# Optimization experiments

Hardware: AMD Instinct MI355X
Metric: run time of the kernel (lower is better)

## Reference

```python
import jax, jax.numpy as jnp
import numpy as np

TOP_K = 2  # moe_top_k


def setup_inputs() -> dict:
    key = jax.random.key(0)
    k0, k1, k2, k3 = jax.random.split(key, 4)
    SL, BS, H, F, E = 2048, 4, 1024, 1024, 8
    x = jax.random.normal(k0, (SL, BS, H), dtype=jnp.float32)
    w_router = jax.random.normal(k1, (H, E), dtype=jnp.float32) * 0.02
    w1 = jax.random.normal(k2, (E, H, F), dtype=jnp.float32) * 0.02  # per-expert map weights
    w2 = jax.random.normal(k3, (E, F, H), dtype=jnp.float32) * 0.02  # per-expert reduce weights
    return {"x": x, "w_router": w_router, "w1": w1, "w2": w2}


def reference(x, w_router, w1, w2):
    # dMoA forward: router -> dropless dispatch -> per-expert map GEMM ->
    # per-expert reduce GEMM -> expert-weighted combine. Dropless = no capacity
    # dropping, so a dense all-experts compute + per-token selection is exactly
    # equivalent in math to the sort/gather/grouped-GEMM/scatter pipeline.
    sl, bs, h = x.shape
    E = w1.shape[0]
    xt = x.reshape(-1, h)  # [T, H], T = sl*bs
    T = xt.shape[0]

    # LearnedRouter: softmax over expert logits, then top-k weights/indices
    scores = jax.nn.softmax(xt @ w_router, axis=-1)       # [T, E]
    expert_weights, top_experts = jax.lax.top_k(scores, TOP_K)  # [T, K]

    # load-balancing loss (router.loss): E * sum_e f_e * p_e
    onehot = jax.nn.one_hot(top_experts, E, dtype=xt.dtype)  # [T, K, E]
    tokens_frac = onehot.sum(axis=(0, 1)) / (T * TOP_K)      # f_e
    probs_mean = scores.mean(axis=0)                         # p_e
    loss = E * jnp.sum(tokens_frac * probs_mean)

    # map: per-expert linear H->F, select the top-k experts' outputs per token
    y_all = jnp.einsum('th,ehf->tef', xt, w1)                 # [T, E, F]
    h_tk = jnp.take_along_axis(y_all, top_experts[:, :, None], axis=1)  # [T, K, F]

    # reduce: weighted scatter-combine, then per-expert linear F->H
    hw = jnp.einsum('tke,tk,tkf->tef', onehot, expert_weights, h_tk)  # [T, E, F]
    out = jnp.einsum('tef,efh->th', hw, w2)                   # [T, H]
    return out.reshape(sl, bs, h), loss
```

## Files before the change

kernel.cpp:

```cpp
#include <hip/hip_runtime.h>
#include <hip/hip_bf16.h>
#include <stdint.h>


#define HD 1024
#define FD 1024
#define EN 8

typedef __attribute__((ext_vector_type(8))) short bf16x8;
typedef __attribute__((ext_vector_type(4))) float f32x4;

__device__ __forceinline__ void gload16(const void* g, void* l) {
    __builtin_amdgcn_global_load_lds(
        (const __attribute__((address_space(1))) unsigned int*)g,
        (__attribute__((address_space(3))) unsigned int*)l, 16, 0, 0);
}

__device__ __forceinline__ ushort f2bf(float v) {
    __hip_bfloat16 h = __float2bfloat16(v);
    return *(ushort*)&h;
}
__device__ __forceinline__ float bf2f(ushort u) {
    unsigned int w = ((unsigned int)u) << 16;
    float f; __builtin_memcpy(&f, &w, 4); return f;
}

__global__ __launch_bounds__(256) void router_kernel(
    const float* __restrict__ x, const float* __restrict__ wrt,
    ushort* __restrict__ xb,
    int* __restrict__ top_e, float* __restrict__ top_w,
    int* __restrict__ counts, float* __restrict__ probsum)
{
    __shared__ int   cnt_s[EN];
    __shared__ float ps_s[EN];
    int tid = threadIdx.x;
    if (tid < EN) { cnt_s[tid] = 0; ps_s[tid] = 0.f; }
    __syncthreads();

    int wid = tid >> 6, lane = tid & 63;
    int t = blockIdx.x * 4 + wid;
    const float4* xr4 = (const float4*)(x + (size_t)t * HD);
    ushort4* xbo = (ushort4*)(xb + (size_t)t * HD);
    float acc[EN];
#pragma unroll
    for (int e = 0; e < EN; e++) acc[e] = 0.f;
#pragma unroll
    for (int it = 0; it < 4; it++) {
        float4 xv = xr4[it * 64 + lane];
        ushort4 o; o.x = f2bf(xv.x); o.y = f2bf(xv.y); o.z = f2bf(xv.z); o.w = f2bf(xv.w);
        xbo[it * 64 + lane] = o;
        int h0 = it * 256 + lane * 4;
        float xs[4] = {xv.x, xv.y, xv.z, xv.w};
#pragma unroll
        for (int j = 0; j < 4; j++) {
            const float4* wp = (const float4*)(wrt + (size_t)(h0 + j) * EN);
            float4 wa = wp[0], wb = wp[1];
            acc[0] += xs[j] * wa.x; acc[1] += xs[j] * wa.y;
            acc[2] += xs[j] * wa.z; acc[3] += xs[j] * wa.w;
            acc[4] += xs[j] * wb.x; acc[5] += xs[j] * wb.y;
            acc[6] += xs[j] * wb.z; acc[7] += xs[j] * wb.w;
        }
    }
#pragma unroll
    for (int off = 32; off >= 1; off >>= 1) {
#pragma unroll
        for (int e = 0; e < EN; e++) acc[e] += __shfl_xor(acc[e], off, 64);
    }
    if (lane == 0) {
        float m = acc[0];
#pragma unroll
        for (int e = 1; e < EN; e++) m = fmaxf(m, acc[e]);
        float p[EN], s = 0.f;
#pragma unroll
        for (int e = 0; e < EN; e++) { p[e] = expf(acc[e] - m); s += p[e]; }
        float inv = 1.f / s;
#pragma unroll
        for (int e = 0; e < EN; e++) p[e] *= inv;
        int e0 = 0;
#pragma unroll
        for (int e = 1; e < EN; e++) if (p[e] > p[e0]) e0 = e;
        int e1 = (e0 == 0) ? 1 : 0;
#pragma unroll
        for (int e = 0; e < EN; e++) {
            if (e == e0) continue;
            if (p[e] > p[e1]) e1 = e;
        }
        top_e[t * 2] = e0;  top_e[t * 2 + 1] = e1;
        top_w[t * 2] = p[e0]; top_w[t * 2 + 1] = p[e1];
        atomicAdd(&cnt_s[e0], 1); atomicAdd(&cnt_s[e1], 1);
#pragma unroll
        for (int e = 0; e < EN; e++) atomicAdd(&ps_s[e], p[e]);
    }
    __syncthreads();
    if (tid < EN) {
        atomicAdd(&counts[tid], cnt_s[tid]);
        atomicAdd(&probsum[tid], ps_s[tid]);
    }
}

__global__ void prep_kernel(const int* __restrict__ counts,
                            const float* __restrict__ probsum,
                            int* __restrict__ offs, float* __restrict__ loss_out)
{
    int off = 0; float loss = 0.f;
    for (int e = 0; e < EN; e++) {
        offs[e] = off;
        off += counts[e];
        loss += ((float)counts[e] / 16384.f) * (probsum[e] / 8192.f);
    }
    offs[EN] = off;
    *loss_out = 8.f * loss;
}

__global__ __launch_bounds__(256) void dispatch_kernel(
    const int* __restrict__ top_e, const float* __restrict__ top_w,
    const int* __restrict__ offs, int* __restrict__ cursor,
    int* __restrict__ tok_list, float* __restrict__ w_list)
{
    int t = blockIdx.x * 256 + threadIdx.x;
    int lane = threadIdx.x & 63;
#pragma unroll
    for (int k = 0; k < 2; k++) {
        int e = top_e[t * 2 + k];
        int idx = 0;
#pragma unroll
        for (int ex = 0; ex < EN; ex++) {
            unsigned long long m = __ballot(e == ex);
            if (e == ex) {
                int cnt = __popcll(m);
                int leader = __ffsll(m) - 1;
                int pos = 0;
                if (lane == leader) pos = atomicAdd(&cursor[ex * 16], cnt);
                pos = __shfl(pos, leader, 64);
                int rank = __popcll(m & ((1ull << lane) - 1ull));
                idx = offs[ex] + pos + rank;
            }
        }
        tok_list[idx] = t * 2 + k;
        w_list[idx] = top_w[t * 2 + k];
    }
}

__global__ __launch_bounds__(256) void transpose_conv_kernel(
    const float* __restrict__ w1, const float* __restrict__ w2,
    ushort* __restrict__ w1b, ushort* __restrict__ w2b)
{
    __shared__ float tile[32][33];
    int bid = blockIdx.x;
    const float* in; ushort* outp;
    if (bid >= 8192) { in = w2; outp = w2b; bid -= 8192; }
    else             { in = w1; outp = w1b; }
    int e  = bid >> 10;
    int t2 = bid & 1023;
    int tb = t2 >> 5;
    int ta = t2 & 31;
    const float* pin = in + ((size_t)e << 20);
    ushort* pout = outp + ((size_t)e << 20);
    int tx = threadIdx.x & 31, ty = threadIdx.x >> 5;
#pragma unroll
    for (int j = 0; j < 4; j++)
        tile[ty + j * 8][tx] = pin[(size_t)(ta * 32 + ty + j * 8) * 1024 + tb * 32 + tx];
    __syncthreads();
#pragma unroll
    for (int j = 0; j < 4; j++)
        pout[(size_t)(tb * 32 + ty + j * 8) * 1024 + ta * 32 + tx] =
            f2bf(tile[tx][ty + j * 8]);
}


__global__ __launch_bounds__(256) void map_gemm(
    const ushort* __restrict__ xb, const ushort* __restrict__ w1b,
    ushort* __restrict__ hbuf,
    const int* __restrict__ tok_list, const float* __restrict__ w_list,
    const int* __restrict__ offs)
{
    __shared__ __align__(16) short lA[128][64];
    __shared__ __align__(16) short lB[128][64];
    __shared__ int   tok_s[128];
    __shared__ float wt_s[128];

    int g = blockIdx.x;
    int e = g & 7, q = g >> 3, nb = q & 7, rb = q >> 3;
    int base = offs[e], cnt = offs[e + 1] - base;
    int row0 = rb << 7;
    if (row0 >= cnt) return;
    int rem = cnt - row0;
    int tid = threadIdx.x;
    if (tid < 128) {
        int r = row0 + tid; if (r > cnt - 1) r = cnt - 1;
        tok_s[tid] = tok_list[base + r];
        wt_s[tid]  = w_list[base + r];
    }
    __syncthreads();

    int lane = tid & 63, w = tid >> 6;
    int wm = w >> 1, wn = w & 1;
    int lo = lane & 15, hi = lane >> 4, rx = lane & 7;

    int lr = lane >> 3;
    int kseg = ((lane & 7) ^ lr) << 3;
    const ushort* pA[4]; const ushort* pB[4];
    const ushort* wbase = w1b + ((size_t)e << 20);
#pragma unroll
    for (int i = 0; i < 4; i++) {
        int rowT = w * 32 + i * 8 + lr;
        pA[i] = xb + (size_t)(tok_s[rowT] >> 1) * HD + kseg;
        pB[i] = wbase + (size_t)(nb * 128 + rowT) * HD + kseg;
    }

    f32x4 acc[4][4];
#pragma unroll
    for (int m = 0; m < 4; m++)
#pragma unroll
        for (int n = 0; n < 4; n++) acc[m][n] = (f32x4){0.f, 0.f, 0.f, 0.f};

    for (int kt = 0; kt < 16; ++kt) {
#pragma unroll
        for (int i = 0; i < 4; i++) {
            int rowT = w * 32 + i * 8 + lr;
            gload16(pA[i], &lA[rowT][0]);
            gload16(pB[i], &lB[rowT][0]);
            pA[i] += 64; pB[i] += 64;
        }
        __syncthreads();
        bf16x8 af[4][2], bg[4][2];
#pragma unroll
        for (int m = 0; m < 4; m++)
#pragma unroll
            for (int ks = 0; ks < 2; ks++)
                af[m][ks] = *(const bf16x8*)&lA[wm * 64 + m * 16 + lo][((ks * 4 + hi) ^ rx) << 3];
#pragma unroll
        for (int n = 0; n < 4; n++)
#pragma unroll
            for (int ks = 0; ks < 2; ks++)
                bg[n][ks] = *(const bf16x8*)&lB[wn * 64 + n * 16 + lo][((ks * 4 + hi) ^ rx) << 3];
#pragma unroll
        for (int ks = 0; ks < 2; ks++)
#pragma unroll
            for (int m = 0; m < 4; m++)
#pragma unroll
                for (int n = 0; n < 4; n++)
                    acc[m][n] = __builtin_amdgcn_mfma_f32_16x16x32_bf16(af[m][ks], bg[n][ks], acc[m][n], 0, 0, 0);
        __syncthreads();
    }

    short* ep = ((short*)lA) + w * 4096;
#pragma unroll
    for (int m = 0; m < 4; m++)
#pragma unroll
        for (int r = 0; r < 4; r++) {
            int row_l = m * 16 + hi * 4 + r;
            int rswz = (row_l & 7) << 4;
            float wgt = wt_s[wm * 64 + row_l];
#pragma unroll
            for (int n = 0; n < 4; n++) {
                int colb = (n * 16 + lo) * 2;
                ep[(row_l * 128 + (colb ^ rswz)) >> 1] = f2bf(acc[m][n][r] * wgt);
            }
        }
    __syncthreads();
    size_t outbase = (size_t)(base + row0);
    int colg0 = (nb << 7) + wn * 64;
#pragma unroll
    for (int j = 0; j < 8; j++) {
        int row_l = j * 8 + (lane >> 3);
        int r_blk = wm * 64 + row_l;
        int sb = ((lane & 7) * 16) ^ ((row_l & 7) << 4);
        bf16x8 v = *(const bf16x8*)&ep[(row_l * 128 + sb) >> 1];
        if (r_blk < rem)
            *(bf16x8*)&hbuf[(outbase + r_blk) * FD + colg0 + (lane & 7) * 8] = v;
    }
}

__global__ __launch_bounds__(256) void reduce_gemm(
    const ushort* __restrict__ hbuf, const ushort* __restrict__ w2b,
    ushort* __restrict__ obuf,
    const int* __restrict__ tok_list, const int* __restrict__ offs)
{
    __shared__ __align__(16) short lA[128][64];
    __shared__ __align__(16) short lB[128][64];
    __shared__ int tok_s[128];

    int g = blockIdx.x;
    int e = g & 7, q = g >> 3, nb = q & 7, rb = q >> 3;
    int base = offs[e], cnt = offs[e + 1] - base;
    int row0 = rb << 7;
    if (row0 >= cnt) return;
    int rem = cnt - row0;
    int tid = threadIdx.x;
    if (tid < 128) {
        int r = row0 + tid; if (r > cnt - 1) r = cnt - 1;
        tok_s[tid] = tok_list[base + r];
    }
    __syncthreads();

    int lane = tid & 63, w = tid >> 6;
    int wm = w >> 1, wn = w & 1;
    int lo = lane & 15, hi = lane >> 4, rx = lane & 7;

    int lr = lane >> 3;
    int kseg = ((lane & 7) ^ lr) << 3;
    const ushort* pA[4]; const ushort* pB[4];
    const ushort* wbase = w2b + ((size_t)e << 20);
#pragma unroll
    for (int i = 0; i < 4; i++) {
        int rowT = w * 32 + i * 8 + lr;
        int ar = row0 + rowT; if (ar > cnt - 1) ar = cnt - 1;
        pA[i] = hbuf + (size_t)(base + ar) * FD + kseg;
        pB[i] = wbase + (size_t)(nb * 128 + rowT) * FD + kseg;
    }

    f32x4 acc[4][4];
#pragma unroll
    for (int m = 0; m < 4; m++)
#pragma unroll
        for (int n = 0; n < 4; n++) acc[m][n] = (f32x4){0.f, 0.f, 0.f, 0.f};

    for (int kt = 0; kt < 16; ++kt) {
#pragma unroll
        for (int i = 0; i < 4; i++) {
            int rowT = w * 32 + i * 8 + lr;
            gload16(pA[i], &lA[rowT][0]);
            gload16(pB[i], &lB[rowT][0]);
            pA[i] += 64; pB[i] += 64;
        }
        __syncthreads();
        bf16x8 af[4][2], bg[4][2];
#pragma unroll
        for (int m = 0; m < 4; m++)
#pragma unroll
            for (int ks = 0; ks < 2; ks++)
                af[m][ks] = *(const bf16x8*)&lA[wm * 64 + m * 16 + lo][((ks * 4 + hi) ^ rx) << 3];
#pragma unroll
        for (int n = 0; n < 4; n++)
#pragma unroll
            for (int ks = 0; ks < 2; ks++)
                bg[n][ks] = *(const bf16x8*)&lB[wn * 64 + n * 16 + lo][((ks * 4 + hi) ^ rx) << 3];
#pragma unroll
        for (int ks = 0; ks < 2; ks++)
#pragma unroll
            for (int m = 0; m < 4; m++)
#pragma unroll
                for (int n = 0; n < 4; n++)
                    acc[m][n] = __builtin_amdgcn_mfma_f32_16x16x32_bf16(af[m][ks], bg[n][ks], acc[m][n], 0, 0, 0);
        __syncthreads();
    }

    short* ep = ((short*)lA) + w * 4096;
#pragma unroll
    for (int m = 0; m < 4; m++)
#pragma unroll
        for (int r = 0; r < 4; r++) {
            int row_l = m * 16 + hi * 4 + r;
            int rswz = (row_l & 7) << 4;
#pragma unroll
            for (int n = 0; n < 4; n++) {
                int colb = (n * 16 + lo) * 2;
                ep[(row_l * 128 + (colb ^ rswz)) >> 1] = f2bf(acc[m][n][r]);
            }
        }
    __syncthreads();
    int colg0 = (nb << 7) + wn * 64;
#pragma unroll
    for (int j = 0; j < 8; j++) {
        int row_l = j * 8 + (lane >> 3);
        int r_blk = wm * 64 + row_l;
        int sb = ((lane & 7) * 16) ^ ((row_l & 7) << 4);
        bf16x8 v = *(const bf16x8*)&ep[(row_l * 128 + sb) >> 1];
        if (r_blk < rem)
            *(bf16x8*)&obuf[(size_t)tok_s[r_blk] * HD + colg0 + (lane & 7) * 8] = v;
    }
}

__global__ __launch_bounds__(256) void combine_kernel(
    const ushort* __restrict__ obuf, float* __restrict__ out)
{
    int g = blockIdx.x * 256 + threadIdx.x;
    int t = g >> 7, c8 = (g & 127) << 3;
    const ushort* p = obuf + (size_t)t * 2048 + c8;
    bf16x8 a = *(const bf16x8*)p;
    bf16x8 b = *(const bf16x8*)(p + 1024);
    float o[8];
#pragma unroll
    for (int i = 0; i < 8; i++)
        o[i] = bf2f((ushort)a[i]) + bf2f((ushort)b[i]);
    float* q = out + (size_t)t * HD + c8;
    *(float4*)q       = (float4){o[0], o[1], o[2], o[3]};
    *(float4*)(q + 4) = (float4){o[4], o[5], o[6], o[7]};
}

extern "C" void kernel_launch(void* const* d_in, const int* in_sizes, int n_in,
                              void* d_out, int out_size, void* d_ws, size_t ws_size,
                              hipStream_t stream)
{
    const float* x   = (const float*)d_in[0];
    const float* wrt = (const float*)d_in[1];
    const float* w1  = (const float*)d_in[2];
    const float* w2  = (const float*)d_in[3];
    float* out = (float*)d_out;

    uint8_t* ws = (uint8_t*)d_ws;
    ushort* xb   = (ushort*)(ws);
    ushort* w1b  = (ushort*)(ws + (16u << 20));
    ushort* obuf = (ushort*)(ws);
    ushort* w2b  = (ushort*)(ws + (32u << 20));
    ushort* hbuf = (ushort*)(ws + (48u << 20));
    uint8_t* p80 = ws + (80u << 20);
    int*   tok_list = (int*)(p80);
    float* w_list   = (float*)(p80 + (64u << 10));
    int*   top_e    = (int*)(p80 + (128u << 10));
    float* top_w    = (float*)(p80 + (192u << 10));
    uint8_t* ctr    = p80 + (256u << 10);
    int*   counts   = (int*)(ctr);
    float* probsum  = (float*)(ctr + 64);
    int*   offs     = (int*)(ctr + 128);
    int*   cursor   = (int*)(ctr + 256);
    float* loss_out = out + 8388608;

    hipMemsetAsync(ctr, 0, 1024, stream);

    router_kernel<<<2048, 256, 0, stream>>>(x, wrt, xb, top_e, top_w, counts, probsum);
    prep_kernel<<<1, 1, 0, stream>>>(counts, probsum, offs, loss_out);
    dispatch_kernel<<<32, 256, 0, stream>>>(top_e, top_w, offs, cursor, tok_list, w_list);
    transpose_conv_kernel<<<16384, 256, 0, stream>>>(w1, w2, w1b, w2b);
    map_gemm<<<1152, 256, 0, stream>>>(xb, w1b, hbuf, tok_list, w_list, offs);
    reduce_gemm<<<1152, 256, 0, stream>>>(hbuf, w2b, obuf, tok_list, offs);
    combine_kernel<<<4096, 256, 0, stream>>>(obuf, out);
}
```

Baseline: 205.6 us.

## Fuse weight transpose into router kernel and fold prep into dispatch

Merges the weight transpose/bf16 conversion and the router into a single launch whose first 8192 blocks convert weights using 64x32 tiles with float4 loads and 16-byte stores, and whose remaining blocks do routing. The single-thread prep kernel is removed; every dispatch thread recomputes expert offsets from the counts, and block 0 writes offsets and the loss. This cuts two kernel launches and widens memory accesses in the transpose. The cost is redundant offset computation in dispatch and a larger shared-memory footprint for the router blocks.

```diff
diff --git a/kernel.cpp b/kernel.cpp
--- a/kernel.cpp
+++ b/kernel.cpp
@@ -25,20 +25,53 @@
     float f; __builtin_memcpy(&f, &w, 4); return f;
 }
 
-__global__ __launch_bounds__(256) void router_kernel(
+__global__ __launch_bounds__(256) void fused_rt_kernel(
     const float* __restrict__ x, const float* __restrict__ wrt,
-    ushort* __restrict__ xb,
+    const float* __restrict__ w1, const float* __restrict__ w2,
+    ushort* __restrict__ xb, ushort* __restrict__ w1b, ushort* __restrict__ w2b,
     int* __restrict__ top_e, float* __restrict__ top_w,
     int* __restrict__ counts, float* __restrict__ probsum)
 {
+    __shared__ float smem[64 * 33];
+    int bid = blockIdx.x;
+    int tid = threadIdx.x;
+
+    if (bid < 8192) {
+        const float* in; ushort* outp;
+        if (bid >= 4096) { in = w2; outp = w2b; bid -= 4096; }
+        else             { in = w1; outp = w1b; }
+        int e  = bid >> 9;
+        int t2 = bid & 511;
+        int kt = t2 >> 5;
+        int nt = t2 & 31;
+        const float* pin = in + ((size_t)e << 20) + (size_t)(kt * 64) * 1024 + nt * 32;
+        ushort* pout = outp + ((size_t)e << 20) + (size_t)(nt * 32) * 1024 + kt * 64;
+#pragma unroll
+        for (int s = 0; s < 2; s++) {
+            int slot = s * 256 + tid;
+            int kk = slot >> 3, c4 = slot & 7;
+            float4 v = *(const float4*)(pin + (size_t)kk * 1024 + c4 * 4);
+            float* d = &smem[kk * 33 + c4 * 4];
+            d[0] = v.x; d[1] = v.y; d[2] = v.z; d[3] = v.w;
+        }
+        __syncthreads();
+        {
+            int n = tid >> 3, ks = (tid & 7) * 8;
+            ushort us[8];
+#pragma unroll
+            for (int i = 0; i < 8; i++) us[i] = f2bf(smem[(ks + i) * 33 + n]);
+            *(uint4*)(pout + (size_t)n * 1024 + ks) = *(uint4*)us;
+        }
+        return;
+    }
+
     __shared__ int   cnt_s[EN];
     __shared__ float ps_s[EN];
-    int tid = threadIdx.x;
     if (tid < EN) { cnt_s[tid] = 0; ps_s[tid] = 0.f; }
     __syncthreads();
 
     int wid = tid >> 6, lane = tid & 63;
-    int t = blockIdx.x * 4 + wid;
+    int t = (bid - 8192) * 4 + wid;
     const float4* xr4 = (const float4*)(x + (size_t)t * HD);
     ushort4* xbo = (ushort4*)(xb + (size_t)t * HD);
     float acc[EN];
@@ -98,25 +131,26 @@
     }
 }
 
-__global__ void prep_kernel(const int* __restrict__ counts,
-                            const float* __restrict__ probsum,
-                            int* __restrict__ offs, float* __restrict__ loss_out)
-{
-    int off = 0; float loss = 0.f;
-    for (int e = 0; e < EN; e++) {
-        offs[e] = off;
-        off += counts[e];
-        loss += ((float)counts[e] / 16384.f) * (probsum[e] / 8192.f);
-    }
-    offs[EN] = off;
-    *loss_out = 8.f * loss;
-}
-
 __global__ __launch_bounds__(256) void dispatch_kernel(
+    const int* __restrict__ counts, const float* __restrict__ probsum,
     const int* __restrict__ top_e, const float* __restrict__ top_w,
-    const int* __restrict__ offs, int* __restrict__ cursor,
-    int* __restrict__ tok_list, float* __restrict__ w_list)
-{
+    int* __restrict__ cursor, int* __restrict__ tok_list,
+    float* __restrict__ w_list, int* __restrict__ offs_g,
+    float* __restrict__ loss_out)
+{
+    int offs[EN + 1]; offs[0] = 0;
+#pragma unroll
+    for (int e = 0; e < EN; e++) offs[e + 1] = offs[e] + counts[e];
+    if (blockIdx.x == 0 && threadIdx.x == 0) {
+        float loss = 0.f;
+#pragma unroll
+        for (int e = 0; e < EN; e++) {
+            offs_g[e] = offs[e];
+            loss += ((float)counts[e] / 16384.f) * (probsum[e] / 8192.f);
+        }
+        offs_g[EN] = offs[EN];
+        *loss_out = 8.f * loss;
+    }
     int t = blockIdx.x * 256 + threadIdx.x;
     int lane = threadIdx.x & 63;
 #pragma unroll
@@ -139,32 +173,6 @@
         tok_list[idx] = t * 2 + k;
         w_list[idx] = top_w[t * 2 + k];
     }
-}
-
-__global__ __launch_bounds__(256) void transpose_conv_kernel(
-    const float* __restrict__ w1, const float* __restrict__ w2,
-    ushort* __restrict__ w1b, ushort* __restrict__ w2b)
-{
-    __shared__ float tile[32][33];
-    int bid = blockIdx.x;
-    const float* in; ushort* outp;
-    if (bid >= 8192) { in = w2; outp = w2b; bid -= 8192; }
-    else             { in = w1; outp = w1b; }
-    int e  = bid >> 10;
-    int t2 = bid & 1023;
-    int tb = t2 >> 5;
-    int ta = t2 & 31;
-    const float* pin = in + ((size_t)e << 20);
-    ushort* pout = outp + ((size_t)e << 20);
-    int tx = threadIdx.x & 31, ty = threadIdx.x >> 5;
-#pragma unroll
-    for (int j = 0; j < 4; j++)
-        tile[ty + j * 8][tx] = pin[(size_t)(ta * 32 + ty + j * 8) * 1024 + tb * 32 + tx];
-    __syncthreads();
-#pragma unroll
-    for (int j = 0; j < 4; j++)
-        pout[(size_t)(tb * 32 + ty + j * 8) * 1024 + ta * 32 + tx] =
-            f2bf(tile[tx][ty + j * 8]);
 }
 
 
@@ -419,10 +427,10 @@
 
     hipMemsetAsync(ctr, 0, 1024, stream);
 
-    router_kernel<<<2048, 256, 0, stream>>>(x, wrt, xb, top_e, top_w, counts, probsum);
-    prep_kernel<<<1, 1, 0, stream>>>(counts, probsum, offs, loss_out);
-    dispatch_kernel<<<32, 256, 0, stream>>>(top_e, top_w, offs, cursor, tok_list, w_list);
-    transpose_conv_kernel<<<16384, 256, 0, stream>>>(w1, w2, w1b, w2b);
+    fused_rt_kernel<<<10240, 256, 0, stream>>>(x, wrt, w1, w2, xb, w1b, w2b,
+                                               top_e, top_w, counts, probsum);
+    dispatch_kernel<<<32, 256, 0, stream>>>(counts, probsum, top_e, top_w,
+                                            cursor, tok_list, w_list, offs, loss_out);
     map_gemm<<<1152, 256, 0, stream>>>(xb, w1b, hbuf, tok_list, w_list, offs);
     reduce_gemm<<<1152, 256, 0, stream>>>(hbuf, w2b, obuf, tok_list, offs);
     combine_kernel<<<4096, 256, 0, stream>>>(obuf, out);
```

Result: faster. 199.8 us (-2.8%).
